# Kernel tuning notes

Measured on AMD Instinct MI355X. Metric: run time of the kernel, lower is better.

## Reference

```python
import jax, jax.numpy as jnp
import numpy as np

ALPHA = 0.5
N_NODES = 100000
N_EDGES = 1600000
D_IN = 128
D_OUT = 128


def setup_inputs() -> dict:
    key = jax.random.key(0)
    k1, k2, k3, k4, k5, k6 = jax.random.split(key, 6)
    x = jax.random.normal(k1, (N_NODES, D_IN), dtype=jnp.float32)
    edge_index = jax.random.randint(k2, (2, N_EDGES), 0, N_NODES, dtype=jnp.int64)
    # torch Linear default init: U(-1/sqrt(fan_in), 1/sqrt(fan_in)); scale similar here
    s = 1.0 / np.sqrt(D_IN)
    W_src = jax.random.uniform(k3, (D_OUT, D_IN), jnp.float32, -s, s)
    b_src = jax.random.uniform(k4, (D_OUT,), jnp.float32, -s, s)
    W_dst = jax.random.uniform(k5, (D_OUT, D_IN), jnp.float32, -s, s)
    b_dst = jax.random.uniform(k6, (D_OUT,), jnp.float32, -s, s)
    return {"x": x, "edge_index": edge_index, "W_src": W_src, "b_src": b_src,
            "W_dst": W_dst, "b_dst": b_dst}


def _inv_sqrt(deg):
    # deg^{-1/2} with inf -> 0 (isolated nodes)
    return jnp.where(deg > 0, jax.lax.rsqrt(jnp.maximum(deg, 1e-30)), 0.0)


def reference(x, edge_index, W_src, b_src, W_dst, b_dst):
    n = x.shape[0]
    row, col = edge_index[0], edge_index[1]
    ones = jnp.ones(row.shape[0], dtype=x.dtype)
    # degrees of directed adjacency A[row, col] = 1
    deg_out = jax.ops.segment_sum(ones, row, num_segments=n)  # row sums
    deg_in = jax.ops.segment_sum(ones, col, num_segments=n)   # col sums
    # D_out^{-1/2} A D_in^{-1/2} edge weights; transpose norm yields the SAME weights
    w = _inv_sqrt(deg_out)[row] * _inv_sqrt(deg_in)[col]      # [E]
    # adj_norm @ x : aggregate sources (col) into destinations (row)
    agg_fwd = jax.ops.segment_sum(w[:, None] * x[col], row, num_segments=n)  # [N, D_IN]
    # adj_t_norm @ x : aggregate destinations (row) into sources (col)
    agg_bwd = jax.ops.segment_sum(w[:, None] * x[row], col, num_segments=n)  # [N, D_IN]
    out = ALPHA * (agg_fwd @ W_src.T + b_src) + (1.0 - ALPHA) * (agg_bwd @ W_dst.T + b_dst)
    return out
```

## Files before the change

### kernel.cpp

```cpp
#include <hip/hip_runtime.h>
#include <stdint.h>

#define D 128
#define CE 2048
#define CAP 5120

typedef __attribute__((ext_vector_type(8))) __bf16 bf16x8;
typedef __attribute__((ext_vector_type(4))) float floatx4;

union FragU { uint4 u; bf16x8 b; };

__device__ __forceinline__ float bf16_lo(uint32_t u) { return __uint_as_float(u << 16); }
__device__ __forceinline__ float bf16_hi(uint32_t u) { return __uint_as_float(u & 0xffff0000u); }
__device__ __forceinline__ uint16_t f32_to_bf16(float f) {
    uint32_t u = __float_as_uint(f);
    uint32_t r = u + 0x7fffu + ((u >> 16) & 1u);
    return (uint16_t)(r >> 16);
}
__device__ __forceinline__ uint32_t pack2(float a, float b) {
    return (uint32_t)f32_to_bf16(a) | ((uint32_t)f32_to_bf16(b) << 16);
}

__global__ __launch_bounds__(256) void k_init(uint32_t* __restrict__ gcursor, int nb2)
{
    for (int j = threadIdx.x + blockIdx.x * 256; j < nb2; j += gridDim.x * 256)
        gcursor[j] = (uint32_t)j * CAP;
}

__global__ __launch_bounds__(256) void k_part(
    const int* __restrict__ ei, int E, int nbuk,
    uint32_t* __restrict__ gcursor, uint32_t* __restrict__ gpairs)
{
    __shared__ uint32_t cnt[1024];
    __shared__ uint32_t loff[1024];
    __shared__ uint32_t gbase[1024];
    __shared__ uint32_t spair[2 * CE];
    __shared__ uint16_t sbid[2 * CE];
    __shared__ uint32_t ssum[256];
    int nb2 = 2 * nbuk;
    for (int j = threadIdx.x; j < nb2; j += 256) cnt[j] = 0;
    __syncthreads();
    int base = blockIdx.x * CE;
    int lim = min(CE, E - base);
    for (int i = threadIdx.x; i < lim; i += 256) {
        int r = ei[base + i];
        int c = ei[E + base + i];
        atomicAdd(&cnt[r >> 8], 1u);
        atomicAdd(&cnt[nbuk + (c >> 8)], 1u);
    }
    __syncthreads();
    uint32_t v0 = 0, v1 = 0, v2 = 0, v3 = 0;
    int b0 = threadIdx.x * 4;
    if (b0 < nb2)     v0 = cnt[b0];
    if (b0 + 1 < nb2) v1 = cnt[b0 + 1];
    if (b0 + 2 < nb2) v2 = cnt[b0 + 2];
    if (b0 + 3 < nb2) v3 = cnt[b0 + 3];
    uint32_t tsum = v0 + v1 + v2 + v3;
    ssum[threadIdx.x] = tsum;
    __syncthreads();
    for (int off = 1; off < 256; off <<= 1) {
        uint32_t t = (threadIdx.x >= (unsigned)off) ? ssum[threadIdx.x - off] : 0u;
        __syncthreads();
        ssum[threadIdx.x] += t;
        __syncthreads();
    }
    uint32_t run = ssum[threadIdx.x] - tsum;
    if (b0 < nb2)     loff[b0]     = run;
    if (b0 + 1 < nb2) loff[b0 + 1] = run + v0;
    if (b0 + 2 < nb2) loff[b0 + 2] = run + v0 + v1;
    if (b0 + 3 < nb2) loff[b0 + 3] = run + v0 + v1 + v2;
    __syncthreads();
    for (int j = threadIdx.x; j < nb2; j += 256) {
        uint32_t c2 = cnt[j];
        gbase[j] = c2 ? atomicAdd(&gcursor[j], c2) : 0u;
        cnt[j] = loff[j];
    }
    __syncthreads();
    for (int i = threadIdx.x; i < lim; i += 256) {
        int r = ei[base + i];
        int c = ei[E + base + i];
        int bf = r >> 8;
        uint32_t sf = atomicAdd(&cnt[bf], 1u);
        spair[sf] = ((uint32_t)c << 8) | (uint32_t)(r & 255);
        sbid[sf] = (uint16_t)bf;
        int bb = nbuk + (c >> 8);
        uint32_t sb = atomicAdd(&cnt[bb], 1u);
        spair[sb] = ((uint32_t)r << 8) | (uint32_t)(c & 255);
        sbid[sb] = (uint16_t)bb;
    }
    __syncthreads();
    int total = 2 * lim;
    for (int s2 = threadIdx.x; s2 < total; s2 += 256) {
        int b = sbid[s2];
        gpairs[gbase[b] + ((uint32_t)s2 - loff[b])] = spair[s2];
    }
}

__global__ __launch_bounds__(256) void k_build(
    const uint32_t* __restrict__ gpairs, const uint32_t* __restrict__ gcursor,
    int nbuk, int N,
    int* __restrict__ edata, uint32_t* __restrict__ ptrg, uint32_t* __restrict__ degg,
    float* __restrict__ inv_o, float* __restrict__ inv_i)
{
    __shared__ uint32_t hist[256], cur[256], ssum[256];
    int b = blockIdx.x;
    int dir = (b >= nbuk) ? 1 : 0;
    int node0 = (b - dir * nbuk) << 8;
    uint32_t base = (uint32_t)b * CAP;
    uint32_t cnt_b = gcursor[b] - base;
    hist[threadIdx.x] = 0;
    __syncthreads();
    for (uint32_t i = threadIdx.x; i < cnt_b; i += 256)
        atomicAdd(&hist[gpairs[base + i] & 255u], 1u);
    __syncthreads();
    uint32_t h = hist[threadIdx.x];
    ssum[threadIdx.x] = h;
    __syncthreads();
    for (int off = 1; off < 256; off <<= 1) {
        uint32_t t = (threadIdx.x >= (unsigned)off) ? ssum[threadIdx.x - off] : 0u;
        __syncthreads();
        ssum[threadIdx.x] += t;
        __syncthreads();
    }
    uint32_t excl = ssum[threadIdx.x] - h;
    cur[threadIdx.x] = excl;
    int n = node0 + threadIdx.x;
    if (n < N) {
        ptrg[dir * N + n] = base + excl;
        degg[dir * N + n] = h;
        float iv = h ? rsqrtf((float)h) : 0.0f;
        if (dir == 0) inv_o[n] = iv; else inv_i[n] = iv;
    }
    __syncthreads();
    for (uint32_t i = threadIdx.x; i < cnt_b; i += 256) {
        uint32_t e = gpairs[base + i];
        uint32_t pos = atomicAdd(&cur[e & 255u], 1u);
        edata[base + pos] = (int)(e >> 8);
    }
}

__global__ __launch_bounds__(256, 2) void k_mm(
    const float* __restrict__ x,
    const float* __restrict__ Wsrc, const float* __restrict__ Wdst,
    const float* __restrict__ inv_o, const float* __restrict__ inv_i,
    uint16_t* __restrict__ u2b, uint16_t* __restrict__ v2b, int N)
{
    const int lane = threadIdx.x & 63;
    const int m16 = lane & 15;
    const int quad = lane >> 4;
    const int mat = blockIdx.x & 1;
    uint16_t* outb = mat ? v2b : u2b;
    const float* inv = mat ? inv_o : inv_i;
    const float* Wm = mat ? Wdst : Wsrc;

    bf16x8 Bf[8][4];
    #pragma unroll
    for (int ct = 0; ct < 8; ++ct) {
        #pragma unroll
        for (int ks = 0; ks < 4; ++ks) {
            const float4* wr = (const float4*)(Wm + (ct * 16 + m16) * 128 + ks * 32 + quad * 8);
            float4 w0 = wr[0], w1 = wr[1];
            FragU f;
            f.u.x = pack2(0.5f * w0.x, 0.5f * w0.y);
            f.u.y = pack2(0.5f * w0.z, 0.5f * w0.w);
            f.u.z = pack2(0.5f * w1.x, 0.5f * w1.y);
            f.u.w = pack2(0.5f * w1.z, 0.5f * w1.w);
            Bf[ct][ks] = f.b;
        }
    }

    const int ntiles = (N + 15) >> 4;
    const int wslot = (blockIdx.x >> 1) * 4 + (threadIdx.x >> 6);
    const int nslot = (gridDim.x >> 1) * 4;

    for (int t = wslot; t < ntiles; t += nslot) {
        int rowA = t * 16 + m16;
        if (rowA >= N) rowA = N - 1;
        const float4* xr = (const float4*)(x + (long)rowA * 128);
        bf16x8 Af[4];
        #pragma unroll
        for (int ks = 0; ks < 4; ++ks) {
            float4 p0 = xr[ks * 8 + quad * 2];
            float4 p1 = xr[ks * 8 + quad * 2 + 1];
            FragU f;
            f.u.x = pack2(p0.x, p0.y);
            f.u.y = pack2(p0.z, p0.w);
            f.u.z = pack2(p1.x, p1.y);
            f.u.w = pack2(p1.z, p1.w);
            Af[ks] = f.b;
        }
        float iv[4];
        #pragma unroll
        for (int r = 0; r < 4; ++r) {
            int row = t * 16 + quad * 4 + r;
            iv[r] = inv[row < N ? row : 0];
        }
        #pragma unroll
        for (int ct = 0; ct < 8; ++ct) {
            floatx4 acc = {};
            #pragma unroll
            for (int ks = 0; ks < 4; ++ks)
                acc = __builtin_amdgcn_mfma_f32_16x16x32_bf16(Af[ks], Bf[ct][ks], acc, 0, 0, 0);
            #pragma unroll
            for (int r = 0; r < 4; ++r) {
                int row = t * 16 + quad * 4 + r;
                if (row < N)
                    outb[(long)row * 128 + ct * 16 + m16] = f32_to_bf16(acc[r] * iv[r]);
            }
        }
    }
}

__global__ __launch_bounds__(256) void k_gather(
    const uint32_t* __restrict__ u2, const uint32_t* __restrict__ v2,
    const int* __restrict__ edata,
    const uint32_t* __restrict__ ptrg, const uint32_t* __restrict__ degg,
    const float* __restrict__ inv_out, const float* __restrict__ inv_in,
    const float* __restrict__ bsrc, const float* __restrict__ bdst,
    float2* __restrict__ out2, int N, int nStart, int nEnd)
{
    int lane = threadIdx.x & 63;
    int node = nStart + blockIdx.x * 4 + (threadIdx.x >> 6);
    if (node >= nEnd) return;

    uint32_t s0 = ptrg[node],     d0 = degg[node];
    uint32_t s1 = ptrg[N + node], d1 = degg[N + node];

    float fx = 0, fy = 0, bx = 0, by = 0;
    uint32_t k = 0;
    for (; k + 4 <= d0; k += 4) {
        uint32_t p0 = u2[(long)edata[s0 + k]     * 64 + lane];
        uint32_t p1 = u2[(long)edata[s0 + k + 1] * 64 + lane];
        uint32_t p2 = u2[(long)edata[s0 + k + 2] * 64 + lane];
        uint32_t p3 = u2[(long)edata[s0 + k + 3] * 64 + lane];
        fx += bf16_lo(p0) + bf16_lo(p1) + bf16_lo(p2) + bf16_lo(p3);
        fy += bf16_hi(p0) + bf16_hi(p1) + bf16_hi(p2) + bf16_hi(p3);
    }
    for (; k < d0; ++k) {
        uint32_t p = u2[(long)edata[s0 + k] * 64 + lane];
        fx += bf16_lo(p); fy += bf16_hi(p);
    }
    k = 0;
    for (; k + 4 <= d1; k += 4) {
        uint32_t p0 = v2[(long)edata[s1 + k]     * 64 + lane];
        uint32_t p1 = v2[(long)edata[s1 + k + 1] * 64 + lane];
        uint32_t p2 = v2[(long)edata[s1 + k + 2] * 64 + lane];
        uint32_t p3 = v2[(long)edata[s1 + k + 3] * 64 + lane];
        bx += bf16_lo(p0) + bf16_lo(p1) + bf16_lo(p2) + bf16_lo(p3);
        by += bf16_hi(p0) + bf16_hi(p1) + bf16_hi(p2) + bf16_hi(p3);
    }
    for (; k < d1; ++k) {
        uint32_t p = v2[(long)edata[s1 + k] * 64 + lane];
        bx += bf16_lo(p); by += bf16_hi(p);
    }

    float io = inv_out[node], ii = inv_in[node];
    float b0 = 0.5f * (bsrc[2 * lane]     + bdst[2 * lane]);
    float b1 = 0.5f * (bsrc[2 * lane + 1] + bdst[2 * lane + 1]);
    out2[(long)node * 64 + lane] =
        make_float2(io * fx + ii * bx + b0, io * fy + ii * by + b1);
}

extern "C" void kernel_launch(void* const* d_in, const int* in_sizes, int n_in,
                              void* d_out, int out_size, void* d_ws, size_t ws_size,
                              hipStream_t stream) {
    const int N = in_sizes[0] / D;
    const int E = in_sizes[1] / 2;
    const int nbuk = (N + 255) >> 8;
    const int nb2 = 2 * nbuk;

    const float* x    = (const float*)d_in[0];
    const int*   ei   = (const int*)d_in[1];
    const float* Wsrc = (const float*)d_in[2];
    const float* bsrc = (const float*)d_in[3];
    const float* Wdst = (const float*)d_in[4];
    const float* bdst = (const float*)d_in[5];

    char* ws = (char*)d_ws;
    size_t off = 0;
    uint32_t* gcur   = (uint32_t*)(ws + off); off += 1024 * 4;
    float*    inv_o  = (float*)(ws + off);    off += (size_t)N * 4;
    float*    inv_i  = (float*)(ws + off);    off += (size_t)N * 4;
    uint32_t* ptrg   = (uint32_t*)(ws + off); off += (size_t)2 * N * 4;
    uint32_t* degg   = (uint32_t*)(ws + off); off += (size_t)2 * N * 4;
    uint32_t* gpairs = (uint32_t*)(ws + off); off += (size_t)nb2 * CAP * 4;
    int*      edata  = (int*)(ws + off);      off += (size_t)nb2 * CAP * 4;
    uint32_t* u2     = (uint32_t*)(ws + off); off += (size_t)N * 64 * 4;
    uint32_t* v2     = (uint32_t*)(ws + off); off += (size_t)N * 64 * 4;

    k_init<<<4, 256, 0, stream>>>(gcur, nb2);

    k_part<<<(E + CE - 1) / CE, 256, 0, stream>>>(ei, E, nbuk, gcur, gpairs);

    k_build<<<nb2, 256, 0, stream>>>(gpairs, gcur, nbuk, N,
                                     edata, ptrg, degg, inv_o, inv_i);

    k_mm<<<1024, 256, 0, stream>>>(x, Wsrc, Wdst, inv_o, inv_i,
                                   (uint16_t*)u2, (uint16_t*)v2, N);

    int half = (N + 1) / 2;
    k_gather<<<(half + 3) / 4, 256, 0, stream>>>(u2, v2, edata, ptrg, degg,
                                                 inv_o, inv_i, bsrc, bdst,
                                                 (float2*)d_out, N, 0, half);
    k_gather<<<(N - half + 3) / 4, 256, 0, stream>>>(u2, v2, edata, ptrg, degg,
                                                     inv_o, inv_i, bsrc, bdst,
                                                     (float2*)d_out, N, half, N);
}
```

Measured before the change: 366.3 us.

## Stage weights in LDS and swap MFMA operands for packed bf16 row stores

The transform kernel now converts the weight matrix to bf16 fragments once per block into shared memory, replacing the 32 register-held fragments per thread. The MFMA operands are swapped so each lane holds four consecutive output columns of one node, which allows one 8-byte packed store per lane instead of four scattered 2-byte stores, and only one inverse-degree load per tile. The occupancy hint is removed and the grid is doubled. In exchange, every MFMA step now reads from LDS and each block pays a weight-staging prologue.

```diff
diff --git a/kernel.cpp b/kernel.cpp
--- a/kernel.cpp
+++ b/kernel.cpp
@@ -139,45 +139,41 @@
     }
 }
 
-__global__ __launch_bounds__(256, 2) void k_mm(
+__global__ __launch_bounds__(256) void k_mm(
     const float* __restrict__ x,
     const float* __restrict__ Wsrc, const float* __restrict__ Wdst,
     const float* __restrict__ inv_o, const float* __restrict__ inv_i,
-    uint16_t* __restrict__ u2b, uint16_t* __restrict__ v2b, int N)
-{
+    uint32_t* __restrict__ u2, uint32_t* __restrict__ v2, int N)
+{
+    __shared__ uint4 sWf[2048];
     const int lane = threadIdx.x & 63;
     const int m16 = lane & 15;
     const int quad = lane >> 4;
     const int mat = blockIdx.x & 1;
-    uint16_t* outb = mat ? v2b : u2b;
+    uint32_t* outb = mat ? v2 : u2;
     const float* inv = mat ? inv_o : inv_i;
     const float* Wm = mat ? Wdst : Wsrc;
 
-    bf16x8 Bf[8][4];
-    #pragma unroll
-    for (int ct = 0; ct < 8; ++ct) {
-        #pragma unroll
-        for (int ks = 0; ks < 4; ++ks) {
-            const float4* wr = (const float4*)(Wm + (ct * 16 + m16) * 128 + ks * 32 + quad * 8);
-            float4 w0 = wr[0], w1 = wr[1];
-            FragU f;
-            f.u.x = pack2(0.5f * w0.x, 0.5f * w0.y);
-            f.u.y = pack2(0.5f * w0.z, 0.5f * w0.w);
-            f.u.z = pack2(0.5f * w1.x, 0.5f * w1.y);
-            f.u.w = pack2(0.5f * w1.z, 0.5f * w1.w);
-            Bf[ct][ks] = f.b;
+    {
+        uint32_t* sW32 = (uint32_t*)sWf;
+        for (int idx = threadIdx.x; idx < 8192; idx += 256) {
+            int slot = idx >> 2, j2 = idx & 3;
+            int ct = slot >> 8, ks = (slot >> 6) & 3, qd = (slot >> 4) & 3, mm = slot & 15;
+            const float2 w = *(const float2*)(Wm + (ct * 16 + mm) * 128 + ks * 32 + qd * 8 + 2 * j2);
+            sW32[idx] = pack2(0.5f * w.x, 0.5f * w.y);
         }
     }
+    __syncthreads();
 
     const int ntiles = (N + 15) >> 4;
     const int wslot = (blockIdx.x >> 1) * 4 + (threadIdx.x >> 6);
     const int nslot = (gridDim.x >> 1) * 4;
 
     for (int t = wslot; t < ntiles; t += nslot) {
-        int rowA = t * 16 + m16;
-        if (rowA >= N) rowA = N - 1;
+        int node = t * 16 + m16;
+        int rowA = node < N ? node : N - 1;
         const float4* xr = (const float4*)(x + (long)rowA * 128);
-        bf16x8 Af[4];
+        bf16x8 Xf[4];
         #pragma unroll
         for (int ks = 0; ks < 4; ++ks) {
             float4 p0 = xr[ks * 8 + quad * 2];
@@ -187,25 +183,23 @@
             f.u.y = pack2(p0.z, p0.w);
             f.u.z = pack2(p1.x, p1.y);
             f.u.w = pack2(p1.z, p1.w);
-            Af[ks] = f.b;
+            Xf[ks] = f.b;
         }
-        float iv[4];
-        #pragma unroll
-        for (int r = 0; r < 4; ++r) {
-            int row = t * 16 + quad * 4 + r;
-            iv[r] = inv[row < N ? row : 0];
-        }
+        float iv = inv[rowA];
+        bool ok = (node < N);
         #pragma unroll
         for (int ct = 0; ct < 8; ++ct) {
             floatx4 acc = {};
             #pragma unroll
-            for (int ks = 0; ks < 4; ++ks)
-                acc = __builtin_amdgcn_mfma_f32_16x16x32_bf16(Af[ks], Bf[ct][ks], acc, 0, 0, 0);
-            #pragma unroll
-            for (int r = 0; r < 4; ++r) {
-                int row = t * 16 + quad * 4 + r;
-                if (row < N)
-                    outb[(long)row * 128 + ct * 16 + m16] = f32_to_bf16(acc[r] * iv[r]);
+            for (int ks = 0; ks < 4; ++ks) {
+                FragU wf; wf.u = sWf[ct * 256 + ks * 64 + lane];
+                acc = __builtin_amdgcn_mfma_f32_16x16x32_bf16(wf.b, Xf[ks], acc, 0, 0, 0);
+            }
+            if (ok) {
+                uint2 val;
+                val.x = pack2(acc[0] * iv, acc[1] * iv);
+                val.y = pack2(acc[2] * iv, acc[3] * iv);
+                *(uint2*)(outb + (long)node * 64 + ct * 8 + quad * 2) = val;
             }
         }
     }
@@ -295,8 +289,7 @@
     k_build<<<nb2, 256, 0, stream>>>(gpairs, gcur, nbuk, N,
                                      edata, ptrg, degg, inv_o, inv_i);
 
-    k_mm<<<1024, 256, 0, stream>>>(x, Wsrc, Wdst, inv_o, inv_i,
-                                   (uint16_t*)u2, (uint16_t*)v2, N);
+    k_mm<<<2048, 256, 0, stream>>>(x, Wsrc, Wdst, inv_o, inv_i, u2, v2, N);
 
     int half = (N + 1) / 2;
     k_gather<<<(half + 3) / 4, 256, 0, stream>>>(u2, v2, edata, ptrg, degg,
```

After: 347.7 us. 1.05x faster.
